# Kernel optimization log

Hardware: AMD Instinct MI355X
Metric: run time of the kernel (lower is better)

## Reference

```python
import jax, jax.numpy as jnp
import numpy as np

B, TQ, TK, E, H, DH = 4, 1024, 1024, 1024, 16, 64
EPS = 1e-5

def setup_inputs() -> dict:
    key = jax.random.key(0)
    ks = jax.random.split(key, 16)
    s = 0.02
    return {
        "x": jax.random.normal(ks[0], (B, TQ, E), jnp.float32),
        "encoder_out": jax.random.normal(ks[1], (B, TK, E), jnp.float32),
        "Q1w": jax.random.normal(ks[2], (H, DH, E), jnp.float32) * s,
        "Q1b": jax.random.normal(ks[3], (H, DH), jnp.float32) * s,
        "Q2w": jax.random.normal(ks[4], (H, DH, E), jnp.float32) * s,
        "Q2b": jax.random.normal(ks[5], (H, DH), jnp.float32) * s,
        "K1w": jax.random.normal(ks[6], (H, DH, E), jnp.float32) * s,
        "K1b": jax.random.normal(ks[7], (H, DH), jnp.float32) * s,
        "K2w": jax.random.normal(ks[8], (H, DH, E), jnp.float32) * s,
        "K2b": jax.random.normal(ks[9], (H, DH), jnp.float32) * s,
        "Vw": jax.random.normal(ks[10], (H, DH, E), jnp.float32) * s,
        "Vb": jax.random.normal(ks[11], (H, DH), jnp.float32) * s,
        "lam": jax.random.uniform(ks[12], (H,), jnp.float32, 0.5, 1.0),
        "gn_gamma": jnp.ones((H * DH,), jnp.float32),
        "gn_beta": jnp.zeros((H * DH,), jnp.float32),
        "out_w": jax.random.normal(ks[13], (E, H * DH), jnp.float32) * s,
        "out_b": jax.random.normal(ks[14], (E,), jnp.float32) * s,
    }

def _proj(inp, w, b):
    # inp: [B,T,E], w: [H,DH,E] -> [B,H,T,DH]
    return jnp.einsum('bte,hde->bhtd', inp, w) + b[None, :, None, :]

def reference(x, encoder_out, Q1w, Q1b, Q2w, Q2b, K1w, K1b, K2w, K2b, Vw, Vb,
              lam, gn_gamma, gn_beta, out_w, out_b):
    scale = 1.0 / jnp.sqrt(jnp.float32(DH))
    q1 = _proj(x, Q1w, Q1b)
    q2 = _proj(x, Q2w, Q2b)
    k1 = _proj(encoder_out, K1w, K1b)
    k2 = _proj(encoder_out, K2w, K2b)
    v = _proj(encoder_out, Vw, Vb)
    s1 = jnp.einsum('bhtd,bhsd->bhts', q1, k1) * scale  # [B,H,TQ,TK]
    s2 = jnp.einsum('bhtd,bhsd->bhts', q2, k2) * scale
    w = jax.nn.softmax(s1, axis=-1) - lam[None, :, None, None] * jax.nn.softmax(s2, axis=-1)
    out = jnp.einsum('bhts,bhsd->bhtd', w, v)  # [B,H,TQ,DH]
    # GroupNorm(num_groups=H, channels=H*DH) over [B,C,T]: per (B,H) stats over (T,DH)
    mu = jnp.mean(out, axis=(2, 3), keepdims=True)
    var = jnp.mean(jnp.square(out - mu), axis=(2, 3), keepdims=True)
    normed = (out - mu) * jax.lax.rsqrt(var + EPS)
    g = gn_gamma.reshape(H, DH)[None, :, None, :]
    b_ = gn_beta.reshape(H, DH)[None, :, None, :]
    normed = normed * g + b_
    y = normed.transpose(0, 2, 1, 3).reshape(B, TQ, H * DH)
    return y @ out_w.T + out_b
```

## Files before the change

### kernel.cpp

```cpp
#include <hip/hip_runtime.h>
#include <cmath>

typedef __bf16 bf16_t;
typedef bf16_t bf16x8 __attribute__((ext_vector_type(8)));
typedef bf16_t bf16x4 __attribute__((ext_vector_type(4)));
typedef float  f32x4  __attribute__((ext_vector_type(4)));

#define Bn  4
#define TQn 1024
#define TKn 1024
#define En  1024
#define Hn  16
#define DHn 64

static constexpr float EPSv = 1e-5f;
static constexpr float C_SCALE = 0.18033688011112042f;

#define GLDS16(g, l)                                                         \
    __builtin_amdgcn_global_load_lds(                                        \
        (const __attribute__((address_space(1))) void*)(g),                  \
        (__attribute__((address_space(3))) void*)(l), 16, 0, 0)

__global__ __launch_bounds__(256)
void cvt_all(const float* __restrict__ x, const float* __restrict__ enc,
             const float* __restrict__ q1w, const float* __restrict__ q2w,
             const float* __restrict__ k1w, const float* __restrict__ k2w,
             const float* __restrict__ vw,  const float* __restrict__ outw,
             bf16_t* __restrict__ xb, bf16_t* __restrict__ encb,
             bf16_t* __restrict__ wq, bf16_t* __restrict__ wkv,
             bf16_t* __restrict__ wob, float* __restrict__ stats)
{
    if (blockIdx.x == 0 && threadIdx.x < 128) stats[threadIdx.x] = 0.f;
    int idx = blockIdx.x * 256 + threadIdx.x;
    const float* src; bf16_t* dst;
    if      (idx < 1048576) { src = x    + (size_t)idx * 4;              dst = xb   + (size_t)idx * 4; }
    else if (idx < 2097152) { src = enc  + (size_t)(idx - 1048576) * 4;  dst = encb + (size_t)(idx - 1048576) * 4; }
    else if (idx < 2359296) { src = q1w  + (size_t)(idx - 2097152) * 4;  dst = wq   + (size_t)(idx - 2097152) * 4; }
    else if (idx < 2621440) { src = q2w  + (size_t)(idx - 2359296) * 4;  dst = wq   + 1048576 + (size_t)(idx - 2359296) * 4; }
    else if (idx < 2883584) { src = k1w  + (size_t)(idx - 2621440) * 4;  dst = wkv  + (size_t)(idx - 2621440) * 4; }
    else if (idx < 3145728) { src = k2w  + (size_t)(idx - 2883584) * 4;  dst = wkv  + 1048576 + (size_t)(idx - 2883584) * 4; }
    else if (idx < 3407872) { src = vw   + (size_t)(idx - 3145728) * 4;  dst = wkv  + 2097152 + (size_t)(idx - 3145728) * 4; }
    else                    { src = outw + (size_t)(idx - 3407872) * 4;  dst = wob  + (size_t)(idx - 3407872) * 4; }
    float4 v = *(const float4*)src;
    bf16x4 o;
    o[0] = (bf16_t)v.x; o[1] = (bf16_t)v.y; o[2] = (bf16_t)v.z; o[3] = (bf16_t)v.w;
    *(bf16x4*)dst = o;
}

__global__ __launch_bounds__(256, 3)
void gemm_proj(const bf16_t* __restrict__ xb, const bf16_t* __restrict__ encb,
               const bf16_t* __restrict__ wq, const bf16_t* __restrict__ wkv,
               const float* __restrict__ q1b, const float* __restrict__ q2b,
               const float* __restrict__ k1b, const float* __restrict__ k2b,
               const float* __restrict__ vb,
               bf16_t* __restrict__ q12, bf16_t* __restrict__ k12v)
{
    __shared__ bf16_t sA[128 * 64];
    __shared__ bf16_t sB[128 * 64];
    const int tid = threadIdx.x;
    const int w = tid >> 6, lane = tid & 63;
    const int q = lane >> 4, r = lane & 15;
    const int wm = w & 1, wn = w >> 1;
    const int blockM = blockIdx.y * 128, blockN = blockIdx.x * 128;
    const int seg = blockN >> 10;
    const bf16_t* A = (seg < 2) ? xb : encb;
    const bf16_t* W = (seg < 2) ? (wq + (size_t)blockN * 1024)
                                : (wkv + (size_t)(blockN - 2048) * 1024);
    const float* bp = (seg == 0) ? q1b : (seg == 1) ? q2b :
                      (seg == 2) ? k1b : (seg == 3) ? k2b : vb;

    f32x4 acc[4][4];
#pragma unroll
    for (int i = 0; i < 4; ++i)
#pragma unroll
        for (int j = 0; j < 4; ++j) acc[i][j] = (f32x4){0.f, 0.f, 0.f, 0.f};

    for (int k0 = 0; k0 < 1024; k0 += 64) {
#pragma unroll
        for (int c = 0; c < 4; ++c) {
            const int s = c * 256 + tid;
            const int row = s >> 3;
            const int cg = (s & 7) ^ (row & 7);
            GLDS16(A + (size_t)(blockM + row) * 1024 + k0 + cg * 8, sA + c * 2048 + w * 512);
            GLDS16(W + (size_t)row * 1024 + k0 + cg * 8,            sB + c * 2048 + w * 512);
        }
        __syncthreads();
#pragma unroll
        for (int ks = 0; ks < 2; ++ks) {
            bf16x8 a[4], b[4];
#pragma unroll
            for (int i = 0; i < 4; ++i) {
                const int row = wm * 64 + i * 16 + r;
                const int g = (ks * 4 + q) ^ (row & 7);
                a[i] = *(const bf16x8*)&sA[row * 64 + g * 8];
            }
#pragma unroll
            for (int j = 0; j < 4; ++j) {
                const int row = wn * 64 + j * 16 + r;
                const int g = (ks * 4 + q) ^ (row & 7);
                b[j] = *(const bf16x8*)&sB[row * 64 + g * 8];
            }
#pragma unroll
            for (int i = 0; i < 4; ++i)
#pragma unroll
                for (int j = 0; j < 4; ++j)
                    acc[i][j] = __builtin_amdgcn_mfma_f32_16x16x32_bf16(a[i], b[j], acc[i][j], 0, 0, 0);
        }
        __syncthreads();
    }

#pragma unroll
    for (int j = 0; j < 4; ++j) {
        const int n = blockN + wn * 64 + j * 16 + r;
        const int nl = n & 1023;
        const int h = nl >> 6, d = nl & 63;
        const float bv = bp[nl];
#pragma unroll
        for (int i = 0; i < 4; ++i) {
            f32x4 v = acc[i][j];
#pragma unroll
            for (int e = 0; e < 4; ++e) {
                const int m = blockM + wm * 64 + i * 16 + q * 4 + e;
                const int bb = m >> 10, t = m & 1023;
                const float val = v[e] + bv;
                if (seg < 2) {
                    q12[((size_t)(seg * 4 + bb) * 16 + h) * 65536 + (size_t)t * 64 + d] = (bf16_t)val;
                } else if (seg < 4) {
                    k12v[((size_t)((seg - 2) * 4 + bb) * 16 + h) * 65536 + (size_t)t * 64 + d] = (bf16_t)val;
                } else {
                    k12v[((size_t)(8 + bb) * 16 + h) * 65536 + (size_t)d * 1024 + t] = (bf16_t)val;
                }
            }
        }
    }
}

__global__ __launch_bounds__(256, 3)
void gemm_out(const bf16_t* __restrict__ A, const bf16_t* __restrict__ W,
              const float* __restrict__ bias, float* __restrict__ C)
{
    __shared__ bf16_t sA[128 * 64];
    __shared__ bf16_t sB[128 * 64];
    const int tid = threadIdx.x;
    const int w = tid >> 6, lane = tid & 63;
    const int q = lane >> 4, r = lane & 15;
    const int wm = w & 1, wn = w >> 1;
    const int blockM = blockIdx.y * 128, blockN = blockIdx.x * 128;

    f32x4 acc[4][4];
#pragma unroll
    for (int i = 0; i < 4; ++i)
#pragma unroll
        for (int j = 0; j < 4; ++j) acc[i][j] = (f32x4){0.f, 0.f, 0.f, 0.f};

    for (int k0 = 0; k0 < 1024; k0 += 64) {
#pragma unroll
        for (int c = 0; c < 4; ++c) {
            const int s = c * 256 + tid;
            const int row = s >> 3;
            const int cg = (s & 7) ^ (row & 7);
            GLDS16(A + (size_t)(blockM + row) * 1024 + k0 + cg * 8, sA + c * 2048 + w * 512);
            GLDS16(W + (size_t)(blockN + row) * 1024 + k0 + cg * 8, sB + c * 2048 + w * 512);
        }
        __syncthreads();
#pragma unroll
        for (int ks = 0; ks < 2; ++ks) {
            bf16x8 a[4], b[4];
#pragma unroll
            for (int i = 0; i < 4; ++i) {
                const int row = wm * 64 + i * 16 + r;
                const int g = (ks * 4 + q) ^ (row & 7);
                a[i] = *(const bf16x8*)&sA[row * 64 + g * 8];
            }
#pragma unroll
            for (int j = 0; j < 4; ++j) {
                const int row = wn * 64 + j * 16 + r;
                const int g = (ks * 4 + q) ^ (row & 7);
                b[j] = *(const bf16x8*)&sB[row * 64 + g * 8];
            }
#pragma unroll
            for (int i = 0; i < 4; ++i)
#pragma unroll
                for (int j = 0; j < 4; ++j)
                    acc[i][j] = __builtin_amdgcn_mfma_f32_16x16x32_bf16(a[i], b[j], acc[i][j], 0, 0, 0);
        }
        __syncthreads();
    }

#pragma unroll
    for (int j = 0; j < 4; ++j) {
        const int n = blockN + wn * 64 + j * 16 + r;
        const float bv = bias[n];
#pragma unroll
        for (int i = 0; i < 4; ++i) {
            f32x4 v = acc[i][j];
#pragma unroll
            for (int e = 0; e < 4; ++e) {
                const int m = blockM + wm * 64 + i * 16 + q * 4 + e;
                C[(size_t)m * 1024 + n] = v[e] + bv;
            }
        }
    }
}

__global__ __launch_bounds__(512, 4)
void diff_attn_mfma(const bf16_t* __restrict__ q12, const bf16_t* __restrict__ k12v,
                    const float* __restrict__ lam, bf16_t* __restrict__ out,
                    float* __restrict__ stats)
{
    __shared__ bf16_t sK1[64 * 64];
    __shared__ bf16_t sK2[64 * 64];
    __shared__ bf16_t sVt[64 * 64];
    __shared__ bf16_t sPt[128 * 64];

    const int tid = threadIdx.x;
    const int w = tid >> 6, lane = tid & 63;
    const int q = lane >> 4, r = lane & 15;
    const int bh = blockIdx.x, qt = blockIdx.y;
    const float lamv = lam[bh & (Hn - 1)];

    const size_t HT = (size_t)TKn * DHn;
    const bf16_t* q1g = q12 + (size_t)bh * HT + ((size_t)qt * 128 + w * 16) * 64;
    const bf16_t* q2g = q1g + 64 * HT;
    const bf16_t* k1g = k12v + (size_t)bh * HT;
    const bf16_t* k2g = k1g + 64 * HT;
    const bf16_t* vg  = k12v + (size_t)(128 + bh) * HT;

    bf16x8 fQ1[2], fQ2[2];
#pragma unroll
    for (int ks = 0; ks < 2; ++ks) {
        fQ1[ks] = *(const bf16x8*)(q1g + (size_t)r * 64 + ks * 32 + q * 8);
        fQ2[ks] = *(const bf16x8*)(q2g + (size_t)r * 64 + ks * 32 + q * 8);
    }

    f32x4 O1[4], O2[4];
    float l1 = 0.f, l2 = 0.f;
#pragma unroll
    for (int j = 0; j < 4; ++j) { O1[j] = (f32x4){0.f,0.f,0.f,0.f}; O2[j] = (f32x4){0.f,0.f,0.f,0.f}; }

    const int srow = tid >> 3;
    const int scg  = (tid & 7) ^ (srow & 7);

    for (int st = 0; st < TKn / 64; ++st) {
        __syncthreads();
        GLDS16(k1g + (size_t)st * 4096 + srow * 64 + scg * 8, sK1 + w * 512);
        GLDS16(k2g + (size_t)st * 4096 + srow * 64 + scg * 8, sK2 + w * 512);
        GLDS16(vg + (size_t)srow * 1024 + st * 64 + scg * 8,  sVt + w * 512);
        __syncthreads();

#pragma unroll
        for (int stream = 0; stream < 2; ++stream) {
            const bf16_t* sK = stream ? sK2 : sK1;
            const bf16x8 (&fQ)[2] = stream ? fQ2 : fQ1;
            f32x4 (&O)[4] = stream ? O2 : O1;

            f32x4 S[4];
#pragma unroll
            for (int i = 0; i < 4; ++i) S[i] = (f32x4){0.f,0.f,0.f,0.f};
#pragma unroll
            for (int ks = 0; ks < 2; ++ks) {
#pragma unroll
                for (int i = 0; i < 4; ++i) {
                    const int g = (ks * 4 + q) ^ (r & 7);
                    bf16x8 fK = *(const bf16x8*)&sK[(i * 16 + r) * 64 + g * 8];
                    S[i] = __builtin_amdgcn_mfma_f32_16x16x32_bf16(fK, fQ[ks], S[i], 0, 0, 0);
                }
            }
            float part = 0.f;
#pragma unroll
            for (int i = 0; i < 4; ++i) {
                bf16x4 pk;
#pragma unroll
                for (int e = 0; e < 4; ++e) {
                    const float p = __builtin_amdgcn_exp2f(S[i][e] * C_SCALE);
                    part += p;
                    pk[e] = (bf16_t)p;
                }
                const int sb = i * 16 + q * 4;
                const int g = (sb >> 3) ^ (r & 7);
                *(bf16x4*)&sPt[(w * 16 + r) * 64 + g * 8 + (sb & 7)] = pk;
            }
            if (stream) l2 += part; else l1 += part;

#pragma unroll
            for (int ks = 0; ks < 2; ++ks) {
                const int g = (ks * 4 + q) ^ (r & 7);
                bf16x8 fP = *(const bf16x8*)&sPt[(w * 16 + r) * 64 + g * 8];
#pragma unroll
                for (int j = 0; j < 4; ++j) {
                    bf16x8 fV = *(const bf16x8*)&sVt[(j * 16 + r) * 64 + g * 8];
                    O[j] = __builtin_amdgcn_mfma_f32_16x16x32_bf16(fP, fV, O[j], 0, 0, 0);
                }
            }
        }
    }

    l1 += __shfl_xor(l1, 16); l1 += __shfl_xor(l1, 32);
    l2 += __shfl_xor(l2, 16); l2 += __shfl_xor(l2, 32);

    bf16_t* op = out + ((size_t)bh * TQn + (size_t)qt * 128 + w * 16) * DHn;
    float ssum = 0.f, ssq = 0.f;
#pragma unroll
    for (int e = 0; e < 4; ++e) {
        const int t_l = q * 4 + e;
        const float inv1 = 1.0f / __shfl(l1, t_l);
        const float inv2 = lamv / __shfl(l2, t_l);
#pragma unroll
        for (int j = 0; j < 4; ++j) {
            const float o = O1[j][e] * inv1 - O2[j][e] * inv2;
            op[(size_t)t_l * 64 + j * 16 + r] = (bf16_t)o;
            ssum += o;
            ssq += o * o;
        }
    }
#pragma unroll
    for (int d = 1; d < 64; d <<= 1) {
        ssum += __shfl_xor(ssum, d);
        ssq  += __shfl_xor(ssq, d);
    }
    if (lane == 0) {
        atomicAdd(&stats[bh], ssum);
        atomicAdd(&stats[64 + bh], ssq);
    }
}

__global__ __launch_bounds__(256)
void gn_apply(const bf16_t* __restrict__ attn, const float* __restrict__ stats,
              const float* __restrict__ gamma, const float* __restrict__ beta,
              bf16_t* __restrict__ y)
{
    const int f = blockIdx.x * 256 + threadIdx.x;
    const int d8 = (f & 7) << 3;
    const int t  = (f >> 3) & 1023;
    const int bh = f >> 13;
    const int h  = bh & 15;
    const int b  = bh >> 4;
    const float s1 = stats[bh], s2 = stats[64 + bh];
    const float mu = s1 * (1.f / 65536.f);
    const float var = s2 * (1.f / 65536.f) - mu * mu;
    const float rstd = rsqrtf(var + EPSv);
    bf16x8 v = *(const bf16x8*)&attn[((size_t)bh << 16) + t * 64 + d8];
    const int c = h * 64 + d8;
    const float* gp = gamma + c;
    const float* bp = beta + c;
    bf16x8 o;
#pragma unroll
    for (int i = 0; i < 8; ++i)
        o[i] = (bf16_t)(((float)v[i] - mu) * rstd * gp[i] + bp[i]);
    *(bf16x8*)&y[((size_t)(b * 1024 + t)) * 1024 + c] = o;
}

extern "C" void kernel_launch(void* const* d_in, const int* in_sizes, int n_in,
                              void* d_out, int out_size, void* d_ws, size_t ws_size,
                              hipStream_t stream)
{
    const float* x    = (const float*)d_in[0];
    const float* enc  = (const float*)d_in[1];
    const float* Q1w  = (const float*)d_in[2];
    const float* Q1b  = (const float*)d_in[3];
    const float* Q2w  = (const float*)d_in[4];
    const float* Q2b  = (const float*)d_in[5];
    const float* K1w  = (const float*)d_in[6];
    const float* K1b  = (const float*)d_in[7];
    const float* K2w  = (const float*)d_in[8];
    const float* K2b  = (const float*)d_in[9];
    const float* Vw   = (const float*)d_in[10];
    const float* Vb   = (const float*)d_in[11];
    const float* lam  = (const float*)d_in[12];
    const float* gng  = (const float*)d_in[13];
    const float* gnb  = (const float*)d_in[14];
    const float* outw = (const float*)d_in[15];
    const float* outb = (const float*)d_in[16];
    float* out = (float*)d_out;

    bf16_t* xb   = (bf16_t*)d_ws;
    bf16_t* encb = xb   + 4194304;
    bf16_t* wq   = encb + 4194304;
    bf16_t* wkv  = wq   + 2097152;
    bf16_t* wob  = wkv  + 3145728;
    bf16_t* q12  = wob  + 1048576;
    bf16_t* k12v = q12  + 8388608;
    bf16_t* yb   = k12v + 12582912;
    bf16_t* attnb= yb   + 4194304;
    float*  stats= (float*)(attnb + 4194304);

    cvt_all<<<14336, 256, 0, stream>>>(x, enc, Q1w, Q2w, K1w, K2w, Vw, outw,
                                       xb, encb, wq, wkv, wob, stats);

    gemm_proj<<<dim3(40, 32), 256, 0, stream>>>(xb, encb, wq, wkv,
                                                Q1b, Q2b, K1b, K2b, Vb,
                                                q12, k12v);

    diff_attn_mfma<<<dim3(64, 8), 512, 0, stream>>>(q12, k12v, lam, attnb, stats);

    gn_apply<<<2048, 256, 0, stream>>>(attnb, stats, gng, gnb, yb);

    gemm_out<<<dim3(8, 32), 256, 0, stream>>>(yb, wob, outb, out);
}
```

Before: 283.3 us.

## Widen conversion, stage projection epilogue via LDS, merge PV MFMAs across streams

The conversion kernel now handles 8 floats per thread with 16-byte bf16 stores, halving the grid. The projection GEMM epilogue writes results into shared memory (transposed for V) and then issues coalesced 16-byte global stores, replacing scattered 2-byte stores. The attention kernel keeps separate per-warp P buffers for both streams and runs a single shared PV loop that reuses each V fragment load for both O1 and O2. Launch bounds for the GEMMs rise to 4 blocks per SM, which may increase register pressure or spilling.

```diff
diff --git a/kernel.cpp b/kernel.cpp
--- a/kernel.cpp
+++ b/kernel.cpp
@@ -33,21 +33,23 @@
     if (blockIdx.x == 0 && threadIdx.x < 128) stats[threadIdx.x] = 0.f;
     int idx = blockIdx.x * 256 + threadIdx.x;
     const float* src; bf16_t* dst;
-    if      (idx < 1048576) { src = x    + (size_t)idx * 4;              dst = xb   + (size_t)idx * 4; }
-    else if (idx < 2097152) { src = enc  + (size_t)(idx - 1048576) * 4;  dst = encb + (size_t)(idx - 1048576) * 4; }
-    else if (idx < 2359296) { src = q1w  + (size_t)(idx - 2097152) * 4;  dst = wq   + (size_t)(idx - 2097152) * 4; }
-    else if (idx < 2621440) { src = q2w  + (size_t)(idx - 2359296) * 4;  dst = wq   + 1048576 + (size_t)(idx - 2359296) * 4; }
-    else if (idx < 2883584) { src = k1w  + (size_t)(idx - 2621440) * 4;  dst = wkv  + (size_t)(idx - 2621440) * 4; }
-    else if (idx < 3145728) { src = k2w  + (size_t)(idx - 2883584) * 4;  dst = wkv  + 1048576 + (size_t)(idx - 2883584) * 4; }
-    else if (idx < 3407872) { src = vw   + (size_t)(idx - 3145728) * 4;  dst = wkv  + 2097152 + (size_t)(idx - 3145728) * 4; }
-    else                    { src = outw + (size_t)(idx - 3407872) * 4;  dst = wob  + (size_t)(idx - 3407872) * 4; }
-    float4 v = *(const float4*)src;
-    bf16x4 o;
-    o[0] = (bf16_t)v.x; o[1] = (bf16_t)v.y; o[2] = (bf16_t)v.z; o[3] = (bf16_t)v.w;
-    *(bf16x4*)dst = o;
-}
-
-__global__ __launch_bounds__(256, 3)
+    if      (idx <  524288) { src = x    + (size_t)idx * 8;              dst = xb   + (size_t)idx * 8; }
+    else if (idx < 1048576) { src = enc  + (size_t)(idx -  524288) * 8;  dst = encb + (size_t)(idx -  524288) * 8; }
+    else if (idx < 1179648) { src = q1w  + (size_t)(idx - 1048576) * 8;  dst = wq   + (size_t)(idx - 1048576) * 8; }
+    else if (idx < 1310720) { src = q2w  + (size_t)(idx - 1179648) * 8;  dst = wq   + 1048576 + (size_t)(idx - 1179648) * 8; }
+    else if (idx < 1441792) { src = k1w  + (size_t)(idx - 1310720) * 8;  dst = wkv  + (size_t)(idx - 1310720) * 8; }
+    else if (idx < 1572864) { src = k2w  + (size_t)(idx - 1441792) * 8;  dst = wkv  + 1048576 + (size_t)(idx - 1441792) * 8; }
+    else if (idx < 1703936) { src = vw   + (size_t)(idx - 1572864) * 8;  dst = wkv  + 2097152 + (size_t)(idx - 1572864) * 8; }
+    else                    { src = outw + (size_t)(idx - 1703936) * 8;  dst = wob  + (size_t)(idx - 1703936) * 8; }
+    float4 a = *(const float4*)src;
+    float4 b = *(const float4*)(src + 4);
+    bf16x8 o;
+    o[0] = (bf16_t)a.x; o[1] = (bf16_t)a.y; o[2] = (bf16_t)a.z; o[3] = (bf16_t)a.w;
+    o[4] = (bf16_t)b.x; o[5] = (bf16_t)b.y; o[6] = (bf16_t)b.z; o[7] = (bf16_t)b.w;
+    *(bf16x8*)dst = o;
+}
+
+__global__ __launch_bounds__(256, 4)
 void gemm_proj(const bf16_t* __restrict__ xb, const bf16_t* __restrict__ encb,
                const bf16_t* __restrict__ wq, const bf16_t* __restrict__ wkv,
                const float* __restrict__ q1b, const float* __restrict__ q2b,
@@ -109,33 +111,54 @@
         __syncthreads();
     }
 
-#pragma unroll
-    for (int j = 0; j < 4; ++j) {
-        const int n = blockN + wn * 64 + j * 16 + r;
-        const int nl = n & 1023;
-        const int h = nl >> 6, d = nl & 63;
-        const float bv = bp[nl];
-#pragma unroll
-        for (int i = 0; i < 4; ++i) {
-            f32x4 v = acc[i][j];
-#pragma unroll
-            for (int e = 0; e < 4; ++e) {
-                const int m = blockM + wm * 64 + i * 16 + q * 4 + e;
-                const int bb = m >> 10, t = m & 1023;
-                const float val = v[e] + bv;
-                if (seg < 2) {
-                    q12[((size_t)(seg * 4 + bb) * 16 + h) * 65536 + (size_t)t * 64 + d] = (bf16_t)val;
-                } else if (seg < 4) {
-                    k12v[((size_t)((seg - 2) * 4 + bb) * 16 + h) * 65536 + (size_t)t * 64 + d] = (bf16_t)val;
-                } else {
-                    k12v[((size_t)(8 + bb) * 16 + h) * 65536 + (size_t)d * 1024 + t] = (bf16_t)val;
-                }
-            }
-        }
-    }
-}
-
-__global__ __launch_bounds__(256, 3)
+    float bv[4];
+#pragma unroll
+    for (int j = 0; j < 4; ++j)
+        bv[j] = bp[(blockN + wn * 64 + j * 16 + r) & 1023];
+
+    bf16_t* rep = ((w & 2) ? sB : sA) + (w & 1) * 4096;
+    if (seg < 4) {
+#pragma unroll
+        for (int i = 0; i < 4; ++i)
+#pragma unroll
+            for (int j = 0; j < 4; ++j)
+#pragma unroll
+                for (int e = 0; e < 4; ++e)
+                    rep[(i * 16 + q * 4 + e) * 64 + j * 16 + r] = (bf16_t)(acc[i][j][e] + bv[j]);
+    } else {
+#pragma unroll
+        for (int i = 0; i < 4; ++i)
+#pragma unroll
+            for (int j = 0; j < 4; ++j)
+#pragma unroll
+                for (int e = 0; e < 4; ++e)
+                    rep[(j * 16 + r) * 64 + i * 16 + q * 4 + e] = (bf16_t)(acc[i][j][e] + bv[j]);
+    }
+    const int rrow = lane >> 3, rcol = (lane & 7) * 8;
+#pragma unroll
+    for (int t8 = 0; t8 < 8; ++t8) {
+        const int row = t8 * 8 + rrow;
+        bf16x8 v = *(const bf16x8*)&rep[row * 64 + rcol];
+        if (seg < 4) {
+            const int m = blockM + wm * 64 + row;
+            const int bb = m >> 10, t = m & 1023;
+            const int n = blockN + wn * 64 + rcol;
+            const int h = (n >> 6) & 15, d = n & 63;
+            bf16_t* dst = (seg < 2)
+                ? q12  + ((size_t)(seg * 4 + bb) * 16 + h) * 65536 + (size_t)t * 64 + d
+                : k12v + ((size_t)((seg - 2) * 4 + bb) * 16 + h) * 65536 + (size_t)t * 64 + d;
+            *(bf16x8*)dst = v;
+        } else {
+            const int n = blockN + wn * 64 + row;
+            const int h = (n >> 6) & 15, d = n & 63;
+            const int m = blockM + wm * 64 + rcol;
+            const int bb = m >> 10, t = m & 1023;
+            *(bf16x8*)(k12v + ((size_t)(8 + bb) * 16 + h) * 65536 + (size_t)d * 1024 + t) = v;
+        }
+    }
+}
+
+__global__ __launch_bounds__(256, 4)
 void gemm_out(const bf16_t* __restrict__ A, const bf16_t* __restrict__ W,
               const float* __restrict__ bias, float* __restrict__ C)
 {
@@ -211,13 +234,16 @@
     __shared__ bf16_t sK1[64 * 64];
     __shared__ bf16_t sK2[64 * 64];
     __shared__ bf16_t sVt[64 * 64];
-    __shared__ bf16_t sPt[128 * 64];
+    __shared__ bf16_t sP [8 * 2048];
 
     const int tid = threadIdx.x;
     const int w = tid >> 6, lane = tid & 63;
     const int q = lane >> 4, r = lane & 15;
     const int bh = blockIdx.x, qt = blockIdx.y;
     const float lamv = lam[bh & (Hn - 1)];
+
+    bf16_t* sP1 = sP + w * 2048;
+    bf16_t* sP2 = sP1 + 1024;
 
     const size_t HT = (size_t)TKn * DHn;
     const bf16_t* q1g = q12 + (size_t)bh * HT + ((size_t)qt * 128 + w * 16) * 64;
@@ -251,8 +277,8 @@
 #pragma unroll
         for (int stream = 0; stream < 2; ++stream) {
             const bf16_t* sK = stream ? sK2 : sK1;
-            const bf16x8 (&fQ)[2] = stream ? fQ2 : fQ1;
-            f32x4 (&O)[4] = stream ? O2 : O1;
+            const bf16x8* fQ = stream ? fQ2 : fQ1;
+            bf16_t* sPw = stream ? sP2 : sP1;
 
             f32x4 S[4];
 #pragma unroll
@@ -278,19 +304,21 @@
                 }
                 const int sb = i * 16 + q * 4;
                 const int g = (sb >> 3) ^ (r & 7);
-                *(bf16x4*)&sPt[(w * 16 + r) * 64 + g * 8 + (sb & 7)] = pk;
+                *(bf16x4*)&sPw[r * 64 + g * 8 + (sb & 7)] = pk;
             }
             if (stream) l2 += part; else l1 += part;
-
-#pragma unroll
-            for (int ks = 0; ks < 2; ++ks) {
-                const int g = (ks * 4 + q) ^ (r & 7);
-                bf16x8 fP = *(const bf16x8*)&sPt[(w * 16 + r) * 64 + g * 8];
-#pragma unroll
-                for (int j = 0; j < 4; ++j) {
-                    bf16x8 fV = *(const bf16x8*)&sVt[(j * 16 + r) * 64 + g * 8];
-                    O[j] = __builtin_amdgcn_mfma_f32_16x16x32_bf16(fP, fV, O[j], 0, 0, 0);
-                }
+        }
+
+#pragma unroll
+        for (int ks = 0; ks < 2; ++ks) {
+            const int g = (ks * 4 + q) ^ (r & 7);
+            bf16x8 fP1 = *(const bf16x8*)&sP1[r * 64 + g * 8];
+            bf16x8 fP2 = *(const bf16x8*)&sP2[r * 64 + g * 8];
+#pragma unroll
+            for (int j = 0; j < 4; ++j) {
+                bf16x8 fV = *(const bf16x8*)&sVt[(j * 16 + r) * 64 + g * 8];
+                O1[j] = __builtin_amdgcn_mfma_f32_16x16x32_bf16(fP1, fV, O1[j], 0, 0, 0);
+                O2[j] = __builtin_amdgcn_mfma_f32_16x16x32_bf16(fP2, fV, O2[j], 0, 0, 0);
             }
         }
     }
@@ -384,8 +412,8 @@
     bf16_t* attnb= yb   + 4194304;
     float*  stats= (float*)(attnb + 4194304);
 
-    cvt_all<<<14336, 256, 0, stream>>>(x, enc, Q1w, Q2w, K1w, K2w, Vw, outw,
-                                       xb, encb, wq, wkv, wob, stats);
+    cvt_all<<<7168, 256, 0, stream>>>(x, enc, Q1w, Q2w, K1w, K2w, Vw, outw,
+                                      xb, encb, wq, wkv, wob, stats);
 
     gemm_proj<<<dim3(40, 32), 256, 0, stream>>>(xb, encb, wq, wkv,
                                                 Q1b, Q2b, K1b, K2b, Vb,
```

New measurement: 268.8 us. 1.05x faster.
